# Kernel tuning notes

Measured on AMD Instinct MI355X. Metric: run time of the kernel, lower is better.

The kernel has to match this reference:

```python
import jax, jax.numpy as jnp
import numpy as np

N = 50000
E = 400000
IN_DIM = 256
H1, D1 = 4, 128   # gat1: heads=4, hidden=128, concat -> 512
H2, D2 = 1, 64    # gat2: heads=1, out=64, concat=False
NEG_SLOPE = 0.2


def setup_inputs() -> dict:
    key = jax.random.key(0)
    ks = jax.random.split(key, 12)
    x = jax.random.normal(ks[0], (N, IN_DIM), dtype=jnp.float32)
    edge_index = jax.random.randint(ks[1], (2, E), 0, N, dtype=jnp.int64)
    edge_attr = jax.random.normal(ks[2], (E,), dtype=jnp.float32)
    # Glorot-ish init for weights, zeros for biases (as in PyG GATConv)
    def glorot(k, shape):
        fan = shape[0] + shape[-1]
        return jax.random.normal(k, shape, dtype=jnp.float32) * jnp.sqrt(2.0 / fan)
    W1 = glorot(ks[3], (IN_DIM, H1 * D1))
    a1_src = glorot(ks[4], (H1, D1))
    a1_dst = glorot(ks[5], (H1, D1))
    b1 = jnp.zeros((H1 * D1,), dtype=jnp.float32)
    W2 = glorot(ks[6], (H1 * D1, H2 * D2))
    a2_src = glorot(ks[7], (H2, D2))
    a2_dst = glorot(ks[8], (H2, D2))
    b2 = jnp.zeros((D2,), dtype=jnp.float32)
    return {"x": x, "edge_index": edge_index, "edge_attr": edge_attr,
            "W1": W1, "a1_src": a1_src, "a1_dst": a1_dst, "b1": b1,
            "W2": W2, "a2_src": a2_src, "a2_dst": a2_dst, "b2": b2}


def _gat_layer(x, src, dst, W, a_s, a_d, b, heads, d, concat):
    n = x.shape[0]
    h = (x @ W).reshape(n, heads, d)                      # [N,H,D]
    alpha_s = jnp.einsum('nhd,hd->nh', h, a_s)            # [N,H]
    alpha_d = jnp.einsum('nhd,hd->nh', h, a_d)
    e = jax.nn.leaky_relu(alpha_s[src] + alpha_d[dst], NEG_SLOPE)  # [Etot,H]
    # segment softmax over incoming edges of each dst node
    emax = jax.ops.segment_max(e, dst, num_segments=n)
    ex = jnp.exp(e - emax[dst])
    denom = jax.ops.segment_sum(ex, dst, num_segments=n)
    alpha = ex / (denom[dst] + 1e-16)                     # [Etot,H]
    msg = h[src] * alpha[:, :, None]                      # [Etot,H,D]
    out = jax.ops.segment_sum(msg, dst, num_segments=n)   # [N,H,D]
    out = out.reshape(n, heads * d) if concat else out.mean(axis=1)
    return out + b


def reference(x, edge_index, edge_attr, W1, a1_src, a1_dst, b1,
              W2, a2_src, a2_dst, b2):
    # edge_attr is ignored (GATConv built without edge_dim)
    loop = jnp.arange(N, dtype=edge_index.dtype)          # PyG add_self_loops=True
    src = jnp.concatenate([edge_index[0], loop])
    dst = jnp.concatenate([edge_index[1], loop])
    h = _gat_layer(x, src, dst, W1, a1_src, a1_dst, b1, H1, D1, True)
    h = jax.nn.elu(h)
    out = _gat_layer(h, src, dst, W2, a2_src, a2_dst, b2, H2, D2, False)
    return out
```

## Files before the change

### kernel.cpp

```cpp
#include <hip/hip_runtime.h>
#include <cstdint>

typedef unsigned short u16;
typedef short bf16x8_t __attribute__((ext_vector_type(8)));
typedef float f32x4_t __attribute__((ext_vector_type(4)));

#define DEVFN __device__ __forceinline__

DEVFN u16 f2bf(float f) {
  unsigned u = __builtin_bit_cast(unsigned, f);
  u = (u + 0x7fffu + ((u >> 16) & 1u)) >> 16;
  return (u16)u;
}
DEVFN float bf2f(u16 s) {
  unsigned u = ((unsigned)s) << 16;
  return __builtin_bit_cast(float, u);
}

DEVFN void gload_lds16(const u16* g, u16* l) {
  __builtin_amdgcn_global_load_lds(
      (const __attribute__((address_space(1))) void*)g,
      (__attribute__((address_space(3))) void*)l, 16, 0, 0);
}

__global__ void f32_to_bf16_kernel(const float* __restrict__ in, u16* __restrict__ out, long n) {
  long i = ((long)blockIdx.x * 256 + threadIdx.x) * 4;
  if (i + 4 <= n) {
    float4 v = *reinterpret_cast<const float4*>(in + i);
    uint2 pack;
    pack.x = (unsigned)f2bf(v.x) | ((unsigned)f2bf(v.y) << 16);
    pack.y = (unsigned)f2bf(v.z) | ((unsigned)f2bf(v.w) << 16);
    *reinterpret_cast<uint2*>(out + i) = pack;
  }
}

__global__ void conv_w_kernel(const float* __restrict__ W1, const float* __restrict__ W2,
                              u16* __restrict__ w1t, u16* __restrict__ w2t) {
  int idx = blockIdx.x * 256 + threadIdx.x;
  if (idx < 256 * 512) {
    int k = idx / 512, m = idx % 512;
    w1t[m * 256 + k] = f2bf(W1[idx]);
  } else {
    int i2 = idx - 256 * 512;
    if (i2 < 512 * 64) {
      int k = i2 / 64, m = i2 % 64;
      w2t[m * 512 + k] = f2bf(W2[i2]);
    }
  }
}

template<int BM, int BN, int WROWS, int WCOLS, int K, int H, int DH>
__global__ __launch_bounds__(256) void gemm_alpha_kernel(
    const u16* __restrict__ A, const u16* __restrict__ BT, u16* __restrict__ C,
    const float* __restrict__ a_s, const float* __restrict__ a_d,
    float* __restrict__ as_out, float* __restrict__ ad_out, int M, int N)
{
  static_assert(WCOLS == 1 && BN == DH, "alpha store ownership");
  constexpr int BK = 32;
  constexpr int WM = BM / WROWS;
  constexpr int WN = BN / WCOLS;
  constexpr int MF = WM / 16;
  constexpr int NF = WN / 16;
  __shared__ __align__(16) u16 sA[BM][BK];
  __shared__ __align__(16) u16 sB[BN][BK];

  const int tid = threadIdx.x;
  const int lane = tid & 63;
  const int wid = tid >> 6;
  const int wr = wid;
  const int brow = blockIdx.x * BM;
  const int bcol = blockIdx.y * BN;

  f32x4_t acc[MF][NF];
#pragma unroll
  for (int i = 0; i < MF; ++i)
#pragma unroll
    for (int j = 0; j < NF; ++j) acc[i][j] = f32x4_t{0.f, 0.f, 0.f, 0.f};

  const int rsel = lane & 15;
  const int kgrp = (lane >> 4) * 8;
  const int ldrow = tid >> 2;
  const int ldcol = (tid & 3) * 8;

#pragma unroll
  for (int k0 = 0; k0 < K; k0 += BK) {
#pragma unroll
    for (int c = 0; c < BM / 64; ++c) {
      int gr = brow + c * 64 + ldrow; gr = gr < M ? gr : M - 1;
      gload_lds16(A + (size_t)gr * K + k0 + ldcol,
                  &sA[0][0] + c * 2048 + wid * 512);
    }
#pragma unroll
    for (int c = 0; c < BN / 64; ++c) {
      int gb = bcol + c * 64 + ldrow;
      gload_lds16(BT + (size_t)gb * K + k0 + ldcol,
                  &sB[0][0] + c * 2048 + wid * 512);
    }
    __syncthreads();
    bf16x8_t af[MF], bfr[NF];
#pragma unroll
    for (int i = 0; i < MF; ++i)
      af[i] = *reinterpret_cast<const bf16x8_t*>(&sA[wr * WM + i * 16 + rsel][kgrp]);
#pragma unroll
    for (int j = 0; j < NF; ++j)
      bfr[j] = *reinterpret_cast<const bf16x8_t*>(&sB[j * 16 + rsel][kgrp]);
#pragma unroll
    for (int i = 0; i < MF; ++i)
#pragma unroll
      for (int j = 0; j < NF; ++j)
        acc[i][j] = __builtin_amdgcn_mfma_f32_16x16x32_bf16(af[i], bfr[j], acc[i][j], 0, 0, 0);
    __syncthreads();
  }

  const int crow0 = (lane >> 4) * 4;
  const int ccol = lane & 15;

#pragma unroll
  for (int i = 0; i < MF; ++i)
#pragma unroll
    for (int j = 0; j < NF; ++j)
#pragma unroll
      for (int r = 0; r < 4; ++r) {
        int gr = brow + wr * WM + i * 16 + crow0 + r;
        int gc = bcol + j * 16 + ccol;
        if (gr < M) C[(size_t)gr * N + gc] = f2bf(acc[i][j][r]);
      }

  const int head = bcol / DH;
  float asv[NF], adv[NF];
#pragma unroll
  for (int j = 0; j < NF; ++j) {
    int gc = bcol + j * 16 + ccol;
    asv[j] = a_s[gc];
    adv[j] = a_d[gc];
  }
#pragma unroll
  for (int i = 0; i < MF; ++i) {
#pragma unroll
    for (int r = 0; r < 4; ++r) {
      float ps = 0.f, pd = 0.f;
#pragma unroll
      for (int j = 0; j < NF; ++j) {
        float v = acc[i][j][r];
        ps = fmaf(v, asv[j], ps);
        pd = fmaf(v, adv[j], pd);
      }
#pragma unroll
      for (int d = 1; d < 16; d <<= 1) {
        ps += __shfl_xor(ps, d, 64);
        pd += __shfl_xor(pd, d, 64);
      }
      if ((lane & 15) == 0) {
        int gr = brow + wr * WM + i * 16 + crow0 + r;
        if (gr < M) {
          as_out[(size_t)gr * H + head] = ps;
          ad_out[(size_t)gr * H + head] = pd;
        }
      }
    }
  }
}

__global__ void deg_kernel(const int* __restrict__ dst, int* __restrict__ cnt, int e) {
  int i = blockIdx.x * 256 + threadIdx.x;
  if (i < e) atomicAdd(&cnt[dst[i]], 1);
}

DEVFN int block_scan_256(int v, int tid, int* wsum) {
#pragma unroll
  for (int d = 1; d < 64; d <<= 1) {
    int u = __shfl_up(v, d, 64);
    if ((tid & 63) >= d) v += u;
  }
  if ((tid & 63) == 63) wsum[tid >> 6] = v;
  __syncthreads();
  int add = 0;
#pragma unroll
  for (int w = 0; w < 4; ++w) add += (w < (tid >> 6)) ? wsum[w] : 0;
  __syncthreads();
  return v + add;
}

__global__ __launch_bounds__(256) void scan_a_kernel(const int* __restrict__ cnt, int* __restrict__ bsum, int n) {
  __shared__ int ws4[4];
  int i = blockIdx.x * 256 + threadIdx.x;
  int v = (i < n) ? cnt[i] + 1 : 0;
  int incl = block_scan_256(v, threadIdx.x, ws4);
  if (threadIdx.x == 255) bsum[blockIdx.x] = incl;
}

__global__ __launch_bounds__(256) void scan_b_kernel(const int* __restrict__ bsum, int* __restrict__ boff, int nb) {
  __shared__ int ws4[4];
  int v = (threadIdx.x < nb) ? bsum[threadIdx.x] : 0;
  int incl = block_scan_256(v, threadIdx.x, ws4);
  if (threadIdx.x < nb) boff[threadIdx.x] = incl - v;
}

__global__ __launch_bounds__(256) void scan_c_kernel(
    const int* __restrict__ cnt, const int* __restrict__ boff,
    int* __restrict__ rowoff, int* __restrict__ cursor, int n)
{
  __shared__ int ws4[4];
  int i = blockIdx.x * 256 + threadIdx.x;
  int v = (i < n) ? cnt[i] + 1 : 0;
  int incl = block_scan_256(v, threadIdx.x, ws4);
  int excl = incl - v;
  int off = boff[blockIdx.x] + excl;
  if (i < n) {
    rowoff[i] = off;
    cursor[i] = off;
    if (i == n - 1) rowoff[n] = off + v;
  }
}

__global__ void scatter_kernel(const int* __restrict__ srcs, const int* __restrict__ dsts,
                               int* __restrict__ cursor, int* __restrict__ csr, int e, int n) {
  int i = blockIdx.x * 256 + threadIdx.x;
  if (i >= e + n) return;
  int s, d;
  if (i < e) { s = srcs[i]; d = dsts[i]; }
  else       { s = i - e; d = s; }
  int pos = atomicAdd(&cursor[d], 1);
  csr[pos] = s;
}

__global__ __launch_bounds__(256) void agg1_kernel(
    const u16* __restrict__ h1, const float* __restrict__ as1,
    const float* __restrict__ ad1, const int* __restrict__ rowoff,
    const int* __restrict__ csr, const float* __restrict__ b1,
    u16* __restrict__ out, int n)
{
  int node = (blockIdx.x * 256 + threadIdx.x) >> 6;
  int lane = threadIdx.x & 63;
  if (node >= n) return;
  const unsigned head = lane >> 4;
  const unsigned dimbase = lane * 8;
  int e0 = rowoff[node], e1 = rowoff[node + 1];
  float advn = ad1[((unsigned)node << 2) + head];

  float acc[8];
#pragma unroll
  for (int j = 0; j < 8; ++j) acc[j] = 0.f;
  float den = 0.f;

  for (int e = e0; e < e1; ++e) {
    unsigned s = (unsigned)csr[e];
    float t = as1[(s << 2) + head] + advn;
    float l = fmaxf(t, 0.2f * t);
    float ex = __expf(l);
    den += ex;
    bf16x8_t hv = *reinterpret_cast<const bf16x8_t*>(h1 + ((s << 9) + dimbase));
#pragma unroll
    for (int j = 0; j < 8; ++j) acc[j] = fmaf(ex, bf2f((u16)hv[j]), acc[j]);
  }

  float inv = 1.f / (den + 1e-16f);
  u16* orow = out + (((unsigned)node << 9) + dimbase);
#pragma unroll
  for (int j = 0; j < 8; ++j) {
    float v = acc[j] * inv + b1[dimbase + j];
    v = v > 0.f ? v : expm1f(v);
    orow[j] = f2bf(v);
  }
}

__global__ __launch_bounds__(256) void agg2_kernel(
    const u16* __restrict__ h2, const float* __restrict__ as2,
    const float* __restrict__ ad2, const int* __restrict__ rowoff,
    const int* __restrict__ csr, const float* __restrict__ b2,
    float* __restrict__ out, int n)
{
  int node = (blockIdx.x * 256 + threadIdx.x) >> 6;
  int lane = threadIdx.x & 63;
  if (node >= n) return;
  int e0 = rowoff[node], e1 = rowoff[node + 1];
  float advn = ad2[node];

  float acc = 0.f, den = 0.f;
  for (int e = e0; e < e1; ++e) {
    unsigned s = (unsigned)csr[e];
    float t = as2[s] + advn;
    float l = fmaxf(t, 0.2f * t);
    float ex = __expf(l);
    den += ex;
    acc = fmaf(ex, bf2f(h2[(s << 6) + (unsigned)lane]), acc);
  }
  out[((unsigned)node << 6) + lane] = acc / (den + 1e-16f) + b2[lane];
}

extern "C" void kernel_launch(void* const* d_in, const int* in_sizes, int n_in,
                              void* d_out, int out_size, void* d_ws, size_t ws_size,
                              hipStream_t stream) {
  const float* x   = (const float*)d_in[0];
  const int*   ei  = (const int*)d_in[1];
  const float* W1  = (const float*)d_in[3];
  const float* a1s = (const float*)d_in[4];
  const float* a1d = (const float*)d_in[5];
  const float* b1  = (const float*)d_in[6];
  const float* W2  = (const float*)d_in[7];
  const float* a2s = (const float*)d_in[8];
  const float* a2d = (const float*)d_in[9];
  const float* b2  = (const float*)d_in[10];
  float* out = (float*)d_out;

  const int IN_DIM = 256, H1D1 = 512, D2 = 64;
  const int N = in_sizes[0] / IN_DIM;
  const int E = in_sizes[1] / 2;

  char* ws = (char*)d_ws;
  size_t off = 0;
  auto alloc = [&](size_t bytes) -> void* {
    void* p = ws + off;
    off += (bytes + 255) & ~(size_t)255;
    return p;
  };
  u16*  xb     = (u16*)alloc((size_t)N * IN_DIM * 2);
  u16*  w1t    = (u16*)alloc((size_t)H1D1 * IN_DIM * 2);
  u16*  w2t    = (u16*)alloc((size_t)D2 * H1D1 * 2);
  u16*  h1b    = (u16*)alloc((size_t)N * H1D1 * 2);
  int*  cnt    = (int*)alloc((size_t)N * 4);
  float* as1   = (float*)alloc((size_t)N * 4 * 4);
  float* ad1   = (float*)alloc((size_t)N * 4 * 4);
  float* as2   = (float*)alloc((size_t)N * 4);
  float* ad2   = (float*)alloc((size_t)N * 4);
  int*  cursor = (int*)alloc((size_t)N * 4);
  int*  rowoff = (int*)alloc((size_t)(N + 1) * 4);
  int*  bsum   = (int*)alloc(256 * 4);
  int*  boff   = (int*)alloc(256 * 4);
  int*  csr    = (int*)alloc((size_t)(E + N) * 4);
  u16*  h1o    = (u16*)alloc((size_t)N * H1D1 * 2);
  u16*  h2b    = (u16*)alloc((size_t)N * D2 * 2);
  (void)n_in; (void)out_size; (void)ws_size;

  const int* esrc = ei;
  const int* edst = ei + E;

  hipMemsetAsync(cnt, 0, (size_t)N * 4, stream);

  f32_to_bf16_kernel<<<((long)N * IN_DIM / 4 + 255) / 256, 256, 0, stream>>>(x, xb, (long)N * IN_DIM);
  conv_w_kernel<<<(256 * 512 + 512 * 64 + 255) / 256, 256, 0, stream>>>(W1, W2, w1t, w2t);

  dim3 g1((N + 127) / 128, H1D1 / 128);
  gemm_alpha_kernel<128, 128, 4, 1, 256, 4, 128><<<g1, 256, 0, stream>>>(
      xb, w1t, h1b, a1s, a1d, as1, ad1, N, H1D1);

  deg_kernel<<<(E + 255) / 256, 256, 0, stream>>>(edst, cnt, E);
  int nsb = (N + 255) / 256;
  scan_a_kernel<<<nsb, 256, 0, stream>>>(cnt, bsum, N);
  scan_b_kernel<<<1, 256, 0, stream>>>(bsum, boff, nsb);
  scan_c_kernel<<<nsb, 256, 0, stream>>>(cnt, boff, rowoff, cursor, N);
  scatter_kernel<<<(E + N + 255) / 256, 256, 0, stream>>>(esrc, edst, cursor, csr, E, N);

  agg1_kernel<<<(N + 3) / 4, 256, 0, stream>>>(h1b, as1, ad1, rowoff, csr, b1, h1o, N);

  dim3 g2((N + 127) / 128, 1);
  gemm_alpha_kernel<128, 64, 4, 1, 512, 1, 64><<<g2, 256, 0, stream>>>(
      h1o, w2t, h2b, a2s, a2d, as2, ad2, N, D2);

  agg2_kernel<<<(N + 3) / 4, 256, 0, stream>>>(h2b, as2, ad2, rowoff, csr, b2, out, N);
}
```

Before: 272.4 us.

## Merge prep kernels, fold scan pass, widen GEMM K tile, vectorize agg2

Folds the x and weight bf16 conversion and the degree count into one prep kernel, and drops the single-block scan_b by having each scan_c block sum the preceding block totals itself. This removes several launches. The GEMM now uses a BK=64 K-tile with two MFMA k-steps per sync, and the second GEMM uses 64-row tiles for more blocks. agg2 uses 32 lanes per node, each loading two bf16 values, which halves the thread count. In exchange, scan_c does redundant prefix work and the GEMM uses more LDS per block.

```diff
diff --git a/kernel.cpp b/kernel.cpp
--- a/kernel.cpp
+++ b/kernel.cpp
@@ -23,51 +23,52 @@
       (__attribute__((address_space(3))) void*)l, 16, 0, 0);
 }
 
-__global__ void f32_to_bf16_kernel(const float* __restrict__ in, u16* __restrict__ out, long n) {
-  long i = ((long)blockIdx.x * 256 + threadIdx.x) * 4;
-  if (i + 4 <= n) {
-    float4 v = *reinterpret_cast<const float4*>(in + i);
-    uint2 pack;
-    pack.x = (unsigned)f2bf(v.x) | ((unsigned)f2bf(v.y) << 16);
-    pack.y = (unsigned)f2bf(v.z) | ((unsigned)f2bf(v.w) << 16);
-    *reinterpret_cast<uint2*>(out + i) = pack;
-  }
-}
-
-__global__ void conv_w_kernel(const float* __restrict__ W1, const float* __restrict__ W2,
-                              u16* __restrict__ w1t, u16* __restrict__ w2t) {
-  int idx = blockIdx.x * 256 + threadIdx.x;
-  if (idx < 256 * 512) {
-    int k = idx / 512, m = idx % 512;
+__global__ void prep_kernel(const float* __restrict__ x, const float* __restrict__ W1,
+                            const float* __restrict__ W2, const int* __restrict__ edst,
+                            u16* __restrict__ xb, u16* __restrict__ w1t, u16* __restrict__ w2t,
+                            int* __restrict__ cnt, long nx, int e) {
+  const int nxb = (int)((nx + 1023) / 1024);
+  int b = blockIdx.x;
+  if (b < nxb) {
+    long i = ((long)b * 256 + threadIdx.x) * 4;
+    if (i + 4 <= nx) {
+      float4 v = *reinterpret_cast<const float4*>(x + i);
+      uint2 pack;
+      pack.x = (unsigned)f2bf(v.x) | ((unsigned)f2bf(v.y) << 16);
+      pack.y = (unsigned)f2bf(v.z) | ((unsigned)f2bf(v.w) << 16);
+      *reinterpret_cast<uint2*>(xb + i) = pack;
+    }
+  } else if (b < nxb + 512) {
+    int idx = (b - nxb) * 256 + threadIdx.x;
+    int k = idx >> 9, m = idx & 511;
     w1t[m * 256 + k] = f2bf(W1[idx]);
+  } else if (b < nxb + 512 + 128) {
+    int idx = (b - nxb - 512) * 256 + threadIdx.x;
+    int k = idx >> 6, m = idx & 63;
+    w2t[m * 512 + k] = f2bf(W2[idx]);
   } else {
-    int i2 = idx - 256 * 512;
-    if (i2 < 512 * 64) {
-      int k = i2 / 64, m = i2 % 64;
-      w2t[m * 512 + k] = f2bf(W2[i2]);
-    }
-  }
-}
-
-template<int BM, int BN, int WROWS, int WCOLS, int K, int H, int DH>
+    int i = (b - nxb - 640) * 256 + threadIdx.x;
+    if (i < e) atomicAdd(&cnt[edst[i]], 1);
+  }
+}
+
+template<int BM, int BN, int WROWS, int K, int BK, int H, int DH>
 __global__ __launch_bounds__(256) void gemm_alpha_kernel(
     const u16* __restrict__ A, const u16* __restrict__ BT, u16* __restrict__ C,
     const float* __restrict__ a_s, const float* __restrict__ a_d,
     float* __restrict__ as_out, float* __restrict__ ad_out, int M, int N)
 {
-  static_assert(WCOLS == 1 && BN == DH, "alpha store ownership");
-  constexpr int BK = 32;
+  static_assert(BN == DH, "alpha store ownership");
   constexpr int WM = BM / WROWS;
-  constexpr int WN = BN / WCOLS;
   constexpr int MF = WM / 16;
-  constexpr int NF = WN / 16;
+  constexpr int NF = BN / 16;
+  constexpr int KK = BK / 32;
   __shared__ __align__(16) u16 sA[BM][BK];
   __shared__ __align__(16) u16 sB[BN][BK];
 
   const int tid = threadIdx.x;
   const int lane = tid & 63;
-  const int wid = tid >> 6;
-  const int wr = wid;
+  const int wr = tid >> 6;
   const int brow = blockIdx.x * BM;
   const int bcol = blockIdx.y * BN;
 
@@ -79,36 +80,42 @@
 
   const int rsel = lane & 15;
   const int kgrp = (lane >> 4) * 8;
-  const int ldrow = tid >> 2;
-  const int ldcol = (tid & 3) * 8;
 
 #pragma unroll
   for (int k0 = 0; k0 < K; k0 += BK) {
-#pragma unroll
-    for (int c = 0; c < BM / 64; ++c) {
-      int gr = brow + c * 64 + ldrow; gr = gr < M ? gr : M - 1;
-      gload_lds16(A + (size_t)gr * K + k0 + ldcol,
-                  &sA[0][0] + c * 2048 + wid * 512);
-    }
-#pragma unroll
-    for (int c = 0; c < BN / 64; ++c) {
-      int gb = bcol + c * 64 + ldrow;
-      gload_lds16(BT + (size_t)gb * K + k0 + ldcol,
-                  &sB[0][0] + c * 2048 + wid * 512);
+    constexpr int RA = BM * BK / 2048;
+#pragma unroll
+    for (int c = 0; c < RA; ++c) {
+      int t = c * 256 + tid;
+      int row = t * 8 / BK;
+      int col = (t * 8) % BK;
+      int gr = brow + row; gr = gr < M ? gr : M - 1;
+      gload_lds16(A + (size_t)gr * K + k0 + col, &sA[0][0] + t * 8);
+    }
+    constexpr int RB = BN * BK / 2048;
+#pragma unroll
+    for (int c = 0; c < RB; ++c) {
+      int t = c * 256 + tid;
+      int row = t * 8 / BK;
+      int col = (t * 8) % BK;
+      gload_lds16(BT + (size_t)(bcol + row) * K + k0 + col, &sB[0][0] + t * 8);
     }
     __syncthreads();
-    bf16x8_t af[MF], bfr[NF];
-#pragma unroll
-    for (int i = 0; i < MF; ++i)
-      af[i] = *reinterpret_cast<const bf16x8_t*>(&sA[wr * WM + i * 16 + rsel][kgrp]);
-#pragma unroll
-    for (int j = 0; j < NF; ++j)
-      bfr[j] = *reinterpret_cast<const bf16x8_t*>(&sB[j * 16 + rsel][kgrp]);
-#pragma unroll
-    for (int i = 0; i < MF; ++i)
+#pragma unroll
+    for (int kk = 0; kk < KK; ++kk) {
+      bf16x8_t af[MF], bfr[NF];
+#pragma unroll
+      for (int i = 0; i < MF; ++i)
+        af[i] = *reinterpret_cast<const bf16x8_t*>(&sA[wr * WM + i * 16 + rsel][kk * 32 + kgrp]);
 #pragma unroll
       for (int j = 0; j < NF; ++j)
-        acc[i][j] = __builtin_amdgcn_mfma_f32_16x16x32_bf16(af[i], bfr[j], acc[i][j], 0, 0, 0);
+        bfr[j] = *reinterpret_cast<const bf16x8_t*>(&sB[j * 16 + rsel][kk * 32 + kgrp]);
+#pragma unroll
+      for (int i = 0; i < MF; ++i)
+#pragma unroll
+        for (int j = 0; j < NF; ++j)
+          acc[i][j] = __builtin_amdgcn_mfma_f32_16x16x32_bf16(af[i], bfr[j], acc[i][j], 0, 0, 0);
+    }
     __syncthreads();
   }
 
@@ -161,11 +168,6 @@
   }
 }
 
-__global__ void deg_kernel(const int* __restrict__ dst, int* __restrict__ cnt, int e) {
-  int i = blockIdx.x * 256 + threadIdx.x;
-  if (i < e) atomicAdd(&cnt[dst[i]], 1);
-}
-
 DEVFN int block_scan_256(int v, int tid, int* wsum) {
 #pragma unroll
   for (int d = 1; d < 64; d <<= 1) {
@@ -189,23 +191,24 @@
   if (threadIdx.x == 255) bsum[blockIdx.x] = incl;
 }
 
-__global__ __launch_bounds__(256) void scan_b_kernel(const int* __restrict__ bsum, int* __restrict__ boff, int nb) {
-  __shared__ int ws4[4];
-  int v = (threadIdx.x < nb) ? bsum[threadIdx.x] : 0;
-  int incl = block_scan_256(v, threadIdx.x, ws4);
-  if (threadIdx.x < nb) boff[threadIdx.x] = incl - v;
-}
-
 __global__ __launch_bounds__(256) void scan_c_kernel(
-    const int* __restrict__ cnt, const int* __restrict__ boff,
+    const int* __restrict__ cnt, const int* __restrict__ bsum,
     int* __restrict__ rowoff, int* __restrict__ cursor, int n)
 {
   __shared__ int ws4[4];
+  __shared__ int ws4b[4];
+  __shared__ int base_sh;
+  int pre = 0;
+  for (int w = threadIdx.x; w < blockIdx.x; w += 256) pre += bsum[w];
+#pragma unroll
+  for (int d = 1; d < 64; d <<= 1) pre += __shfl_xor(pre, d, 64);
+  if ((threadIdx.x & 63) == 0) ws4b[threadIdx.x >> 6] = pre;
+  __syncthreads();
+  if (threadIdx.x == 0) base_sh = ws4b[0] + ws4b[1] + ws4b[2] + ws4b[3];
   int i = blockIdx.x * 256 + threadIdx.x;
   int v = (i < n) ? cnt[i] + 1 : 0;
   int incl = block_scan_256(v, threadIdx.x, ws4);
-  int excl = incl - v;
-  int off = boff[blockIdx.x] + excl;
+  int off = base_sh + incl - v;
   if (i < n) {
     rowoff[i] = off;
     cursor[i] = off;
@@ -270,22 +273,28 @@
     const int* __restrict__ csr, const float* __restrict__ b2,
     float* __restrict__ out, int n)
 {
-  int node = (blockIdx.x * 256 + threadIdx.x) >> 6;
-  int lane = threadIdx.x & 63;
+  int node = (blockIdx.x * 256 + threadIdx.x) >> 5;
+  int l32 = threadIdx.x & 31;
   if (node >= n) return;
   int e0 = rowoff[node], e1 = rowoff[node + 1];
   float advn = ad2[node];
 
-  float acc = 0.f, den = 0.f;
+  float acc0 = 0.f, acc1 = 0.f, den = 0.f;
   for (int e = e0; e < e1; ++e) {
     unsigned s = (unsigned)csr[e];
     float t = as2[s] + advn;
     float l = fmaxf(t, 0.2f * t);
     float ex = __expf(l);
     den += ex;
-    acc = fmaf(ex, bf2f(h2[(s << 6) + (unsigned)lane]), acc);
-  }
-  out[((unsigned)node << 6) + lane] = acc / (den + 1e-16f) + b2[lane];
+    unsigned hv = *reinterpret_cast<const unsigned*>(h2 + (s << 6) + l32 * 2);
+    acc0 = fmaf(ex, bf2f((u16)(hv & 0xffffu)), acc0);
+    acc1 = fmaf(ex, bf2f((u16)(hv >> 16)), acc1);
+  }
+  float inv = 1.f / (den + 1e-16f);
+  float2 o;
+  o.x = acc0 * inv + b2[l32 * 2];
+  o.y = acc1 * inv + b2[l32 * 2 + 1];
+  *reinterpret_cast<float2*>(out + (((size_t)node) << 6) + l32 * 2) = o;
 }
 
 extern "C" void kernel_launch(void* const* d_in, const int* in_sizes, int n_in,
@@ -326,7 +335,6 @@
   int*  cursor = (int*)alloc((size_t)N * 4);
   int*  rowoff = (int*)alloc((size_t)(N + 1) * 4);
   int*  bsum   = (int*)alloc(256 * 4);
-  int*  boff   = (int*)alloc(256 * 4);
   int*  csr    = (int*)alloc((size_t)(E + N) * 4);
   u16*  h1o    = (u16*)alloc((size_t)N * H1D1 * 2);
   u16*  h2b    = (u16*)alloc((size_t)N * D2 * 2);
@@ -337,25 +345,25 @@
 
   hipMemsetAsync(cnt, 0, (size_t)N * 4, stream);
 
-  f32_to_bf16_kernel<<<((long)N * IN_DIM / 4 + 255) / 256, 256, 0, stream>>>(x, xb, (long)N * IN_DIM);
-  conv_w_kernel<<<(256 * 512 + 512 * 64 + 255) / 256, 256, 0, stream>>>(W1, W2, w1t, w2t);
+  long nx = (long)N * IN_DIM;
+  int nxb = (int)((nx + 1023) / 1024);
+  int eb = (E + 255) / 256;
+  prep_kernel<<<nxb + 640 + eb, 256, 0, stream>>>(x, W1, W2, edst, xb, w1t, w2t, cnt, nx, E);
 
   dim3 g1((N + 127) / 128, H1D1 / 128);
-  gemm_alpha_kernel<128, 128, 4, 1, 256, 4, 128><<<g1, 256, 0, stream>>>(
+  gemm_alpha_kernel<128, 128, 4, 256, 64, 4, 128><<<g1, 256, 0, stream>>>(
       xb, w1t, h1b, a1s, a1d, as1, ad1, N, H1D1);
 
-  deg_kernel<<<(E + 255) / 256, 256, 0, stream>>>(edst, cnt, E);
   int nsb = (N + 255) / 256;
   scan_a_kernel<<<nsb, 256, 0, stream>>>(cnt, bsum, N);
-  scan_b_kernel<<<1, 256, 0, stream>>>(bsum, boff, nsb);
-  scan_c_kernel<<<nsb, 256, 0, stream>>>(cnt, boff, rowoff, cursor, N);
+  scan_c_kernel<<<nsb, 256, 0, stream>>>(cnt, bsum, rowoff, cursor, N);
   scatter_kernel<<<(E + N + 255) / 256, 256, 0, stream>>>(esrc, edst, cursor, csr, E, N);
 
   agg1_kernel<<<(N + 3) / 4, 256, 0, stream>>>(h1b, as1, ad1, rowoff, csr, b1, h1o, N);
 
-  dim3 g2((N + 127) / 128, 1);
-  gemm_alpha_kernel<128, 64, 4, 1, 512, 1, 64><<<g2, 256, 0, stream>>>(
+  dim3 g2((N + 63) / 64, 1);
+  gemm_alpha_kernel<64, 64, 4, 512, 64, 1, 64><<<g2, 256, 0, stream>>>(
       h1o, w2t, h2b, a2s, a2d, as2, ad2, N, D2);
 
-  agg2_kernel<<<(N + 3) / 4, 256, 0, stream>>>(h2b, as2, ad2, rowoff, csr, b2, out, N);
-}
+  agg2_kernel<<<((size_t)N * 32 + 255) / 256, 256, 0, stream>>>(h2b, as2, ad2, rowoff, csr, b2, out, N);
+}
```

Measured after the change: 253.8 us. 1.07x faster.
